# Performance work log

Measured on AMD Instinct MI355X. Metric: run time of the kernel, lower is better.

## Reference

```python
import jax, jax.numpy as jnp
import numpy as np

DIM = 96          # adapter bottleneck dim
K = 3             # conv kernel size

def quick_gelu(x):
    return x * jax.nn.sigmoid(1.702 * x)

def setup_inputs() -> dict:
    key = jax.random.key(0)
    ks = jax.random.split(key, 12)
    B, H, W, C = 64, 28, 28, 384
    x   = jax.random.normal(ks[0], (B, H, W, C), jnp.float32)
    # adapter down/up (xavier-ish scale for down; up is zero-init in the
    # original but we use small random so gradients flow in tests)
    Wd  = jax.random.normal(ks[1], (C, DIM), jnp.float32) * 0.05
    bd  = jnp.zeros((DIM,), jnp.float32)
    Wu  = jax.random.normal(ks[2], (DIM, C), jnp.float32) * 0.02
    bu  = jnp.zeros((C,), jnp.float32)
    # meta_net: Linear(C,64) -> ReLU -> Linear(64,64)
    Wm1 = jax.random.normal(ks[3], (C, 64), jnp.float32) * 0.05
    bm1 = jnp.zeros((64,), jnp.float32)
    Wm2 = jax.random.normal(ks[4], (64, 64), jnp.float32) * 0.1
    bm2 = jnp.zeros((64,), jnp.float32)
    # conv hypernet: Linear(64, DIM*DIM*K*K)
    Wh  = jax.random.normal(ks[5], (64, DIM * DIM * K * K), jnp.float32) * 0.01
    bh  = jnp.zeros((DIM * DIM * K * K,), jnp.float32)
    # learned layer embedding
    emb = jax.random.normal(ks[6], (64,), jnp.float32)
    return {"x": x, "Wd": Wd, "bd": bd, "Wm1": Wm1, "bm1": bm1,
            "Wm2": Wm2, "bm2": bm2, "Wh": Wh, "bh": bh, "emb": emb,
            "Wu": Wu, "bu": bu}

def reference(x, Wd, bd, Wm1, bm1, Wm2, bm2, Wh, bh, emb, Wu, bu):
    B, H, W, C = x.shape
    # meta_net(x) then mean over spatial dims -> per-sample prompt feature [B,64]
    h = jax.nn.relu(jnp.einsum('bhwc,cd->bhwd', x, Wm1) + bm1)
    prompt = jnp.mean(jnp.einsum('bhwd,de->bhwe', h, Wm2) + bm2, axis=(1, 2))  # [B,64]
    # hypernet: per-sample dynamic conv weights (fuse_type='add')
    wflat = (emb[None, :] + prompt) @ Wh + bh                 # [B, DIM*DIM*9]
    wconv = wflat.reshape(B * DIM, DIM, K, K)                 # grouped OIHW
    # adapter down + QuickGELU
    xd = quick_gelu(jnp.einsum('bhwc,cd->bhwd', x, Wd) + bd)  # [B,H,W,DIM]
    # fused batched dynamic conv via grouped conv (groups = B)
    xg = xd.transpose(0, 3, 1, 2).reshape(1, B * DIM, H, W)   # [1,B*DIM,H,W]
    yg = jax.lax.conv_general_dilated(
        xg, wconv, window_strides=(1, 1), padding=((1, 1), (1, 1)),
        dimension_numbers=('NCHW', 'OIHW', 'NCHW'), feature_group_count=B)
    y = yg.reshape(B, DIM, H, W).transpose(0, 2, 3, 1)        # [B,H,W,DIM]
    y = quick_gelu(y)  # dropout is identity in eval mode
    return jnp.einsum('bhwd,dc->bhwc', y, Wu) + bu
```

## Files before the change

kernel.cpp:

```cpp
#include <hip/hip_runtime.h>
#include <hip/hip_fp16.h>

#define BATCH 64
#define HH    28
#define WW2   28
#define HWPX  784
#define PTOT  50176
#define CIN   384
#define DIM   96
#define MDIM  64
#define JTOT  82944
#define WSAMP 82944

#define XD_OFF 0u
#define Y_OFF  9633792u
#define WP_OFF 19267584u
#define HS_OFF 29884416u
#define Z_OFF  29900800u
#define WUT_OFF 29917184u

typedef _Float16 f16x8 __attribute__((ext_vector_type(8)));
typedef _Float16 f16x4 __attribute__((ext_vector_type(4)));
typedef float f32x4 __attribute__((ext_vector_type(4)));

__device__ __forceinline__ float qgelu(float v) {
    return v / (1.f + __expf(-1.702f * v));
}

__global__ void k0_wcvt(const float* __restrict__ Wm1,
                        const float* __restrict__ Wd,
                        const float* __restrict__ Wu,
                        _Float16* __restrict__ Wt,
                        _Float16* __restrict__ WuT)
{
    int i = blockIdx.x * 256 + threadIdx.x;
    if (i < 61440) {
        int o = i / CIN, k = i - o * CIN;
        float v = (o < MDIM) ? Wm1[k * MDIM + o] : Wd[k * DIM + (o - MDIM)];
        Wt[i] = (_Float16)v;
    } else {
        int j = i - 61440;
        int c = j / DIM, d = j - c * DIM;
        WuT[j] = (_Float16)Wu[d * CIN + c];
    }
}

__global__ __launch_bounds__(512, 4) void k1_mfma(
    const float* __restrict__ x, const _Float16* __restrict__ Wt,
    const float* __restrict__ bm1, const float* __restrict__ bd,
    float* __restrict__ hsum, __half* __restrict__ xd)
{
    __shared__ char smem[25088];
    _Float16* xds = (_Float16*)smem;
    float*   hred = (float*)(smem + 24576);

    const int t = threadIdx.x;
    const int p0 = blockIdx.x * 128;
    const int lane = t & 63, w = t >> 6;
    const int wm = w >> 1, wn = w & 1;
    const int rl = lane & 15, q = lane >> 4;

    const float* a0 = x + (size_t)(p0 + wm * 32 + rl) * CIN + q * 8;
    const float* a1 = a0 + 16 * CIN;
    const _Float16* bp0 = Wt + (wn * 80 + rl) * CIN + q * 8;

    f32x4 acc[2][5];
    #pragma unroll
    for (int mf = 0; mf < 2; ++mf)
        #pragma unroll
        for (int nf = 0; nf < 5; ++nf) acc[mf][nf] = (f32x4){0.f, 0.f, 0.f, 0.f};

    #pragma unroll
    for (int kc = 0; kc < 12; ++kc) {
        f16x8 bv[5];
        #pragma unroll
        for (int nf = 0; nf < 5; ++nf)
            bv[nf] = *(const f16x8*)(bp0 + nf * 16 * CIN + kc * 32);

        float4 fa0 = *(const float4*)(a0 + kc * 32);
        float4 fa1 = *(const float4*)(a0 + kc * 32 + 4);
        float4 fb0 = *(const float4*)(a1 + kc * 32);
        float4 fb1 = *(const float4*)(a1 + kc * 32 + 4);

        f16x8 av[2];
        av[0][0] = (_Float16)fa0.x; av[0][1] = (_Float16)fa0.y;
        av[0][2] = (_Float16)fa0.z; av[0][3] = (_Float16)fa0.w;
        av[0][4] = (_Float16)fa1.x; av[0][5] = (_Float16)fa1.y;
        av[0][6] = (_Float16)fa1.z; av[0][7] = (_Float16)fa1.w;
        av[1][0] = (_Float16)fb0.x; av[1][1] = (_Float16)fb0.y;
        av[1][2] = (_Float16)fb0.z; av[1][3] = (_Float16)fb0.w;
        av[1][4] = (_Float16)fb1.x; av[1][5] = (_Float16)fb1.y;
        av[1][6] = (_Float16)fb1.z; av[1][7] = (_Float16)fb1.w;

        #pragma unroll
        for (int mf = 0; mf < 2; ++mf)
            #pragma unroll
            for (int nf = 0; nf < 5; ++nf)
                acc[mf][nf] = __builtin_amdgcn_mfma_f32_16x16x32_f16(
                    av[mf], bv[nf], acc[mf][nf], 0, 0, 0);
    }

    if (t < 128) hred[t] = 0.f;
    __syncthreads();

    const int s0 = p0 / HWPX, s_last = (p0 + 127) / HWPX;
    #pragma unroll
    for (int mf = 0; mf < 2; ++mf) {
        #pragma unroll
        for (int nf = 0; nf < 5; ++nf) {
            const int col = wn * 80 + nf * 16 + rl;
            #pragma unroll
            for (int j = 0; j < 4; ++j) {
                const int rr = wm * 32 + mf * 16 + q * 4 + j;
                float v = acc[mf][nf][j];
                if (col < 64) {
                    v = fmaxf(v + bm1[col], 0.f);
                    int sloc = (p0 + rr) / HWPX - s0;
                    atomicAdd(&hred[sloc * 64 + col], v);
                } else {
                    int e = col - 64;
                    xds[rr * 96 + e] = (_Float16)qgelu(v + bd[e]);
                }
            }
        }
    }
    __syncthreads();

    if (t < 128) {
        int sloc = t >> 6, col = t & 63, s = s0 + sloc;
        if (s <= s_last) atomicAdd(&hsum[s * 64 + col], hred[t]);
    }
    #pragma unroll
    for (int i = 0; i < 3; ++i) {
        int e = t + i * 512;
        *(uint4*)((__half*)xd + (size_t)p0 * 96 + e * 8) = *(uint4*)(xds + e * 8);
    }
}

__global__ void k2a_prompt(const float* __restrict__ hsum,
                           const float* __restrict__ Wm2,
                           const float* __restrict__ bm2,
                           const float* __restrict__ emb,
                           float* __restrict__ z)
{
    int idx = blockIdx.x * 256 + threadIdx.x;
    int b = idx >> 6, m = idx & 63;
    float acc = 0.f;
    #pragma unroll 8
    for (int d = 0; d < 64; ++d) acc += hsum[b * 64 + d] * Wm2[d * 64 + m];
    z[idx] = emb[m] + acc * (1.f / 784.f) + bm2[m];
}

__global__ __launch_bounds__(256) void k2b_hyper(
    const float* __restrict__ z, const float* __restrict__ Wh,
    const float* __restrict__ bh, __half* __restrict__ wperm)
{
    __shared__ float zs[4096];
    const int t = threadIdx.x;
    for (int idx = t; idx < 4096; idx += 256) zs[idx] = z[idx];
    const int j = blockIdx.x * 256 + t;
    float wh[64];
    #pragma unroll 8
    for (int m = 0; m < 64; ++m) wh[m] = Wh[(size_t)m * JTOT + j];
    __syncthreads();

    const int o = j / 864, rem = j % 864;
    const int i = rem / 9, t9 = rem % 9;
    const int base = o * 864 + t9 * 96 + i;
    const float bj = bh[j];
    for (int b = 0; b < 64; ++b) {
        float a = bj;
        const float4* zz = (const float4*)(zs + b * 64);
        #pragma unroll
        for (int m4 = 0; m4 < 16; ++m4) {
            float4 v = zz[m4];
            a += v.x * wh[4 * m4] + v.y * wh[4 * m4 + 1] +
                 v.z * wh[4 * m4 + 2] + v.w * wh[4 * m4 + 3];
        }
        wperm[(size_t)b * WSAMP + base] = __float2half(a);
    }
}

__global__ __launch_bounds__(256) void k3_mfma(
    const __half* __restrict__ xd, const __half* __restrict__ wperm,
    __half* __restrict__ y)
{
    __shared__ __half sm[17600];
    const int t = threadIdx.x;

    const int n = blockIdx.x;
    const int xcd = n & 7, jj0 = n >> 3;
    const int b = xcd * 8 + jj0 / 7;
    const int rt = jj0 % 7;
    const int h0 = rt * 4;

    if (t < 16) *(uint4*)(sm + 17472 + t * 8) = uint4{0u, 0u, 0u, 0u};
    for (int idx = t; idx < 2016; idx += 256) {
        int pix = idx / 12, q = idx - pix * 12;
        int r = pix / 28, col = pix - r * 28;
        int g = h0 - 1 + r;
        uint4 v = {0u, 0u, 0u, 0u};
        if ((unsigned)g < 28u)
            v = *(const uint4*)(xd + (size_t)(b * HWPX + g * 28 + col) * 96 + q * 8);
        *(uint4*)(sm + pix * 104 + q * 8) = v;
    }
    __syncthreads();

    const int lane = t & 63, w = t >> 6;
    const int wm = w >> 1, wn = w & 1;
    const int mloc = lane & 15, klo = (lane >> 4) * 8;
    const int base_m = wm * 64;

    int oh_[4], ow_[4]; bool pv[4];
    #pragma unroll
    for (int mf = 0; mf < 4; ++mf) {
        int p = base_m + mf * 16 + mloc;
        pv[mf] = (p < 112);
        int pp = pv[mf] ? p : 0;
        oh_[mf] = pp / 28; ow_[mf] = pp - oh_[mf] * 28;
    }
    const __half* wp = wperm + (size_t)b * WSAMP + (wn * 48 + mloc) * 864 + klo;

    f32x4 acc[4][3];
    #pragma unroll
    for (int mf = 0; mf < 4; ++mf)
        #pragma unroll
        for (int nf = 0; nf < 3; ++nf) acc[mf][nf] = (f32x4){0.f, 0.f, 0.f, 0.f};

    #pragma unroll
    for (int kh = 0; kh < 3; ++kh) {
        #pragma unroll
        for (int kw = 0; kw < 3; ++kw) {
            const int t9 = kh * 3 + kw;
            int abase[4];
            #pragma unroll
            for (int mf = 0; mf < 4; ++mf) {
                int iw = ow_[mf] + kw - 1;
                bool valid = pv[mf] && ((unsigned)iw < 28u);
                abase[mf] = valid ? ((oh_[mf] + kh) * 28 + iw) * 104 + klo
                                  : 17472 + klo;
            }
            #pragma unroll
            for (int ic = 0; ic < 3; ++ic) {
                f16x8 av[4], bv[3];
                #pragma unroll
                for (int nf = 0; nf < 3; ++nf)
                    bv[nf] = *(const f16x8*)(wp + nf * 13824 + t9 * 96 + ic * 32);
                #pragma unroll
                for (int mf = 0; mf < 4; ++mf)
                    av[mf] = *(const f16x8*)(sm + abase[mf] + ic * 32);
                #pragma unroll
                for (int mf = 0; mf < 4; ++mf)
                    #pragma unroll
                    for (int nf = 0; nf < 3; ++nf)
                        acc[mf][nf] = __builtin_amdgcn_mfma_f32_16x16x32_f16(
                            av[mf], bv[nf], acc[mf][nf], 0, 0, 0);
            }
        }
    }
    __syncthreads();

    #pragma unroll
    for (int mf = 0; mf < 4; ++mf) {
        #pragma unroll
        for (int nf = 0; nf < 3; ++nf) {
            const int o = wn * 48 + nf * 16 + mloc;
            #pragma unroll
            for (int j = 0; j < 4; ++j) {
                int p = base_m + mf * 16 + (lane >> 4) * 4 + j;
                if (p < 112)
                    sm[p * 104 + o] = __float2half(qgelu(acc[mf][nf][j]));
            }
        }
    }
    __syncthreads();
    for (int idx = t; idx < 1344; idx += 256) {
        int pix = idx / 12, q = idx - pix * 12;
        *(uint4*)(y + (size_t)(b * HWPX + h0 * 28 + pix) * 96 + q * 8) =
            *(uint4*)(sm + pix * 104 + q * 8);
    }
}

__global__ __launch_bounds__(512, 2) void k4_mfma(
    const __half* __restrict__ y, const _Float16* __restrict__ WuT,
    const float* __restrict__ bu, float* __restrict__ out)
{
    __shared__ __half ys[128 * 104];
    const int t = threadIdx.x;
    const int p0 = blockIdx.x * 128;

    #pragma unroll
    for (int i = 0; i < 3; ++i) {
        int idx = t + i * 512;
        int pix = idx / 12, q = idx - pix * 12;
        *(uint4*)(ys + pix * 104 + q * 8) =
            *(const uint4*)(y + (size_t)(p0 + pix) * 96 + q * 8);
    }

    const int lane = t & 63, w = t >> 6;
    const int wm = w >> 2, wn = w & 3;
    const int mloc = lane & 15, klo = (lane >> 4) * 8;

    float bcol[6];
    #pragma unroll
    for (int nf = 0; nf < 6; ++nf) bcol[nf] = bu[wn * 96 + nf * 16 + mloc];
    __syncthreads();

    f32x4 acc[4][6];
    #pragma unroll
    for (int mf = 0; mf < 4; ++mf)
        #pragma unroll
        for (int nf = 0; nf < 6; ++nf) acc[mf][nf] = (f32x4){0.f, 0.f, 0.f, 0.f};

    #pragma unroll
    for (int kc = 0; kc < 3; ++kc) {
        f16x8 av[4], bv[6];
        #pragma unroll
        for (int nf = 0; nf < 6; ++nf)
            bv[nf] = *(const f16x8*)(WuT + (wn * 96 + nf * 16 + mloc) * 96 + kc * 32 + klo);
        #pragma unroll
        for (int mf = 0; mf < 4; ++mf)
            av[mf] = *(const f16x8*)(ys + (wm * 64 + mf * 16 + mloc) * 104 + kc * 32 + klo);
        #pragma unroll
        for (int mf = 0; mf < 4; ++mf)
            #pragma unroll
            for (int nf = 0; nf < 6; ++nf)
                acc[mf][nf] = __builtin_amdgcn_mfma_f32_16x16x32_f16(
                    av[mf], bv[nf], acc[mf][nf], 0, 0, 0);
    }

    #pragma unroll
    for (int mf = 0; mf < 4; ++mf) {
        #pragma unroll
        for (int nf = 0; nf < 6; ++nf) {
            const int c = wn * 96 + nf * 16 + mloc;
            #pragma unroll
            for (int j = 0; j < 4; ++j) {
                int p = p0 + wm * 64 + mf * 16 + (lane >> 4) * 4 + j;
                out[(size_t)p * CIN + c] = acc[mf][nf][j] + bcol[nf];
            }
        }
    }
}

extern "C" void kernel_launch(void* const* d_in, const int* in_sizes, int n_in,
                              void* d_out, int out_size, void* d_ws, size_t ws_size,
                              hipStream_t stream)
{
    const float* x   = (const float*)d_in[0];
    const float* Wd  = (const float*)d_in[1];
    const float* bd  = (const float*)d_in[2];
    const float* Wm1 = (const float*)d_in[3];
    const float* bm1 = (const float*)d_in[4];
    const float* Wm2 = (const float*)d_in[5];
    const float* bm2 = (const float*)d_in[6];
    const float* Wh  = (const float*)d_in[7];
    const float* bh  = (const float*)d_in[8];
    const float* emb = (const float*)d_in[9];
    const float* Wu  = (const float*)d_in[10];
    const float* bu  = (const float*)d_in[11];
    float* out = (float*)d_out;

    char* ws = (char*)d_ws;
    __half*   xd    = (__half*)(ws + XD_OFF);
    __half*   ybuf  = (__half*)(ws + Y_OFF);
    __half*   wperm = (__half*)(ws + WP_OFF);
    float*    hsum  = (float*)(ws + HS_OFF);
    float*    z     = (float*)(ws + Z_OFF);
    _Float16* Wt    = (_Float16*)(ws + WP_OFF);
    _Float16* WuT   = (_Float16*)(ws + WUT_OFF);

    hipMemsetAsync(hsum, 0, 64 * 64 * sizeof(float), stream);

    k0_wcvt<<<384, 256, 0, stream>>>(Wm1, Wd, Wu, Wt, WuT);
    k1_mfma<<<392, 512, 0, stream>>>(x, Wt, bm1, bd, hsum, xd);
    k2a_prompt<<<16, 256, 0, stream>>>(hsum, Wm2, bm2, emb, z);
    k2b_hyper<<<324, 256, 0, stream>>>(z, Wh, bh, wperm);
    k3_mfma<<<448, 256, 0, stream>>>(xd, wperm, ybuf);
    k4_mfma<<<392, 512, 0, stream>>>(ybuf, WuT, bu, out);
}
```

Measured before the change: 167.9 us.

## Stage k1 GEMM operands through double-buffered LDS with 64-row tiles

The first projection kernel (x times Wm1/Wd) now copies A and B chunks into padded, double-buffered shared memory tiles, prefetching the chunk two steps ahead into registers. Before, each wave read its operands directly from global memory. The block also shrinks from 512 to 256 threads and covers 64 pixels, so twice as many blocks are launched. The aim is to share weight loads across waves and hide global latency, at the cost of extra LDS traffic and a barrier on each k-step.

```diff
diff --git a/kernel.cpp b/kernel.cpp
--- a/kernel.cpp
+++ b/kernel.cpp
@@ -45,24 +45,57 @@
     }
 }
 
-__global__ __launch_bounds__(512, 4) void k1_mfma(
+__global__ __launch_bounds__(256) void k1_mfma(
     const float* __restrict__ x, const _Float16* __restrict__ Wt,
     const float* __restrict__ bm1, const float* __restrict__ bd,
     float* __restrict__ hsum, __half* __restrict__ xd)
 {
-    __shared__ char smem[25088];
+    __shared__ char smem[32768];
+    _Float16* As  = (_Float16*)smem;
+    _Float16* Bs  = (_Float16*)(smem + 9216);
+    float*   hred = (float*)(smem + 32256);
     _Float16* xds = (_Float16*)smem;
-    float*   hred = (float*)(smem + 24576);
 
     const int t = threadIdx.x;
-    const int p0 = blockIdx.x * 128;
+    const int p0 = blockIdx.x * 64;
     const int lane = t & 63, w = t >> 6;
     const int wm = w >> 1, wn = w & 1;
     const int rl = lane & 15, q = lane >> 4;
 
-    const float* a0 = x + (size_t)(p0 + wm * 32 + rl) * CIN + q * 8;
-    const float* a1 = a0 + 16 * CIN;
-    const _Float16* bp0 = Wt + (wn * 80 + rl) * CIN + q * 8;
+    const int arow = t >> 2, acol = (t & 3) * 8;
+    const int brow0 = t >> 2;
+    const int brow1 = (t + 256) >> 2;
+    const int brow2 = (t + 512) >> 2;
+    const int bcol = (t & 3) * 8;
+
+    const float*    ag  = x  + (size_t)(p0 + arow) * CIN + acol;
+    const _Float16* bg0 = Wt + brow0 * CIN + bcol;
+    const _Float16* bg1 = Wt + brow1 * CIN + bcol;
+    const _Float16* bg2 = Wt + brow2 * CIN + bcol;
+
+    float4 ra[2][2];
+    uint4  rb[2][3];
+
+#define LOAD_CHUNK(s, kc_) do {                                   \
+    ra[s][0] = *(const float4*)(ag + (kc_) * 32);                 \
+    ra[s][1] = *(const float4*)(ag + (kc_) * 32 + 4);             \
+    rb[s][0] = *(const uint4*)(bg0 + (kc_) * 32);                 \
+    rb[s][1] = *(const uint4*)(bg1 + (kc_) * 32);                 \
+    if (t < 128) rb[s][2] = *(const uint4*)(bg2 + (kc_) * 32);    \
+} while (0)
+
+#define WRITE_CHUNK(s) do {                                       \
+    f16x8 h;                                                      \
+    h[0] = (_Float16)ra[s][0].x; h[1] = (_Float16)ra[s][0].y;     \
+    h[2] = (_Float16)ra[s][0].z; h[3] = (_Float16)ra[s][0].w;     \
+    h[4] = (_Float16)ra[s][1].x; h[5] = (_Float16)ra[s][1].y;     \
+    h[6] = (_Float16)ra[s][1].z; h[7] = (_Float16)ra[s][1].w;     \
+    *(f16x8*)(As + (s) * 2304 + arow * 36 + acol) = h;            \
+    *(uint4*)(Bs + (s) * 5760 + brow0 * 36 + bcol) = rb[s][0];    \
+    *(uint4*)(Bs + (s) * 5760 + brow1 * 36 + bcol) = rb[s][1];    \
+    if (t < 128)                                                  \
+        *(uint4*)(Bs + (s) * 5760 + brow2 * 36 + bcol) = rb[s][2];\
+} while (0)
 
     f32x4 acc[2][5];
     #pragma unroll
@@ -70,27 +103,23 @@
         #pragma unroll
         for (int nf = 0; nf < 5; ++nf) acc[mf][nf] = (f32x4){0.f, 0.f, 0.f, 0.f};
 
+    LOAD_CHUNK(0, 0);
+    WRITE_CHUNK(0);
+    LOAD_CHUNK(1, 1);
+    __syncthreads();
+
     #pragma unroll
     for (int kc = 0; kc < 12; ++kc) {
-        f16x8 bv[5];
+        const int cur = kc & 1;
+
+        f16x8 av[2], bv[5];
+        av[0] = *(f16x8*)(As + cur * 2304 + (wm * 32 + rl) * 36 + q * 8);
+        av[1] = *(f16x8*)(As + cur * 2304 + (wm * 32 + 16 + rl) * 36 + q * 8);
         #pragma unroll
         for (int nf = 0; nf < 5; ++nf)
-            bv[nf] = *(const f16x8*)(bp0 + nf * 16 * CIN + kc * 32);
-
-        float4 fa0 = *(const float4*)(a0 + kc * 32);
-        float4 fa1 = *(const float4*)(a0 + kc * 32 + 4);
-        float4 fb0 = *(const float4*)(a1 + kc * 32);
-        float4 fb1 = *(const float4*)(a1 + kc * 32 + 4);
-
-        f16x8 av[2];
-        av[0][0] = (_Float16)fa0.x; av[0][1] = (_Float16)fa0.y;
-        av[0][2] = (_Float16)fa0.z; av[0][3] = (_Float16)fa0.w;
-        av[0][4] = (_Float16)fa1.x; av[0][5] = (_Float16)fa1.y;
-        av[0][6] = (_Float16)fa1.z; av[0][7] = (_Float16)fa1.w;
-        av[1][0] = (_Float16)fb0.x; av[1][1] = (_Float16)fb0.y;
-        av[1][2] = (_Float16)fb0.z; av[1][3] = (_Float16)fb0.w;
-        av[1][4] = (_Float16)fb1.x; av[1][5] = (_Float16)fb1.y;
-        av[1][6] = (_Float16)fb1.z; av[1][7] = (_Float16)fb1.w;
+            bv[nf] = *(f16x8*)(Bs + cur * 5760 + (wn * 80 + nf * 16 + rl) * 36 + q * 8);
+
+        if (kc + 2 < 12) LOAD_CHUNK(cur, kc + 2);
 
         #pragma unroll
         for (int mf = 0; mf < 2; ++mf)
@@ -98,12 +127,20 @@
             for (int nf = 0; nf < 5; ++nf)
                 acc[mf][nf] = __builtin_amdgcn_mfma_f32_16x16x32_f16(
                     av[mf], bv[nf], acc[mf][nf], 0, 0, 0);
-    }
-
+
+        if (kc + 1 < 12) {
+            WRITE_CHUNK(cur ^ 1);
+            __syncthreads();
+        }
+    }
+#undef LOAD_CHUNK
+#undef WRITE_CHUNK
+
+    __syncthreads();
     if (t < 128) hred[t] = 0.f;
     __syncthreads();
 
-    const int s0 = p0 / HWPX, s_last = (p0 + 127) / HWPX;
+    const int s0 = p0 / HWPX, s_last = (p0 + 63) / HWPX;
     #pragma unroll
     for (int mf = 0; mf < 2; ++mf) {
         #pragma unroll
@@ -132,7 +169,7 @@
     }
     #pragma unroll
     for (int i = 0; i < 3; ++i) {
-        int e = t + i * 512;
+        int e = t + i * 256;
         *(uint4*)((__half*)xd + (size_t)p0 * 96 + e * 8) = *(uint4*)(xds + e * 8);
     }
 }
@@ -373,7 +410,7 @@
     hipMemsetAsync(hsum, 0, 64 * 64 * sizeof(float), stream);
 
     k0_wcvt<<<384, 256, 0, stream>>>(Wm1, Wd, Wu, Wt, WuT);
-    k1_mfma<<<392, 512, 0, stream>>>(x, Wt, bm1, bd, hsum, xd);
+    k1_mfma<<<784, 256, 0, stream>>>(x, Wt, bm1, bd, hsum, xd);
     k2a_prompt<<<16, 256, 0, stream>>>(hsum, Wm2, bm2, emb, z);
     k2b_hyper<<<324, 256, 0, stream>>>(z, Wh, bh, wperm);
     k3_mfma<<<448, 256, 0, stream>>>(xd, wperm, ybuf);
```

After: 181.1 us. 7.9% more time.

## Stage k1 GEMM operands through double-buffered LDS and split N across blocks

Applied to the files above, without the earlier changes.

Restructures the first projection GEMM so that A (x, converted to fp16) and B tiles are staged through double-buffered shared memory, with a three-deep register prefetch of global loads. The old version loaded operands straight from global into registers. The 160 output columns are now split across two blocks per 128-row tile, doubling the grid to 784 blocks so each wave does one M fragment. The aim is better memory latency hiding and occupancy. The cost is that each x tile is now read twice (once per column half) and there is a barrier on every k-step.

```diff
diff --git a/kernel.cpp b/kernel.cpp
--- a/kernel.cpp
+++ b/kernel.cpp
@@ -50,90 +50,122 @@
     const float* __restrict__ bm1, const float* __restrict__ bd,
     float* __restrict__ hsum, __half* __restrict__ xd)
 {
-    __shared__ char smem[25088];
+    __shared__ char smem[30464];
+    _Float16* As  = (_Float16*)smem;
+    _Float16* Bs  = (_Float16*)(smem + 18432);
+    float*   hred = (float*)(smem + 29952);
     _Float16* xds = (_Float16*)smem;
-    float*   hred = (float*)(smem + 24576);
 
     const int t = threadIdx.x;
-    const int p0 = blockIdx.x * 128;
+    const int bid = blockIdx.x;
+    const int mt = bid >> 1, nb = bid & 1;
+    const int p0 = mt * 128;
+    const int ncol0 = nb * 80;
+
     const int lane = t & 63, w = t >> 6;
-    const int wm = w >> 1, wn = w & 1;
     const int rl = lane & 15, q = lane >> 4;
 
-    const float* a0 = x + (size_t)(p0 + wm * 32 + rl) * CIN + q * 8;
-    const float* a1 = a0 + 16 * CIN;
-    const _Float16* bp0 = Wt + (wn * 80 + rl) * CIN + q * 8;
-
-    f32x4 acc[2][5];
-    #pragma unroll
-    for (int mf = 0; mf < 2; ++mf)
-        #pragma unroll
-        for (int nf = 0; nf < 5; ++nf) acc[mf][nf] = (f32x4){0.f, 0.f, 0.f, 0.f};
+    const int arow = t >> 2, acol = (t & 3) * 8;
+    const float* ag = x + (size_t)(p0 + arow) * CIN + acol;
+    const bool bact = (t < 320);
+    const int brow = t >> 2, bcol = (t & 3) * 8;
+    const _Float16* bg = Wt + (size_t)(ncol0 + (bact ? brow : 0)) * CIN + bcol;
+
+    float4 ra[3][2];
+    uint4  rb[3];
+
+#define LOADC(s, kc_) do {                                        \
+    ra[s][0] = *(const float4*)(ag + (kc_) * 32);                 \
+    ra[s][1] = *(const float4*)(ag + (kc_) * 32 + 4);             \
+    if (bact) rb[s] = *(const uint4*)(bg + (kc_) * 32);           \
+} while (0)
+
+#define WRITEC(buf, s) do {                                       \
+    f16x8 h;                                                      \
+    h[0] = (_Float16)ra[s][0].x; h[1] = (_Float16)ra[s][0].y;     \
+    h[2] = (_Float16)ra[s][0].z; h[3] = (_Float16)ra[s][0].w;     \
+    h[4] = (_Float16)ra[s][1].x; h[5] = (_Float16)ra[s][1].y;     \
+    h[6] = (_Float16)ra[s][1].z; h[7] = (_Float16)ra[s][1].w;     \
+    *(f16x8*)(As + (buf) * 4608 + arow * 36 + acol) = h;          \
+    if (bact)                                                     \
+        *(uint4*)(Bs + (buf) * 2880 + brow * 36 + bcol) = rb[s];  \
+} while (0)
+
+    f32x4 acc[5];
+    #pragma unroll
+    for (int nf = 0; nf < 5; ++nf) acc[nf] = (f32x4){0.f, 0.f, 0.f, 0.f};
+
+    LOADC(0, 0); LOADC(1, 1); LOADC(2, 2);
+    WRITEC(0, 0);
+    __syncthreads();
 
     #pragma unroll
     for (int kc = 0; kc < 12; ++kc) {
+        const int cur = kc & 1;
+
+        f16x8 av = *(f16x8*)(As + cur * 4608 + (w * 16 + rl) * 36 + q * 8);
         f16x8 bv[5];
         #pragma unroll
         for (int nf = 0; nf < 5; ++nf)
-            bv[nf] = *(const f16x8*)(bp0 + nf * 16 * CIN + kc * 32);
-
-        float4 fa0 = *(const float4*)(a0 + kc * 32);
-        float4 fa1 = *(const float4*)(a0 + kc * 32 + 4);
-        float4 fb0 = *(const float4*)(a1 + kc * 32);
-        float4 fb1 = *(const float4*)(a1 + kc * 32 + 4);
-
-        f16x8 av[2];
-        av[0][0] = (_Float16)fa0.x; av[0][1] = (_Float16)fa0.y;
-        av[0][2] = (_Float16)fa0.z; av[0][3] = (_Float16)fa0.w;
-        av[0][4] = (_Float16)fa1.x; av[0][5] = (_Float16)fa1.y;
-        av[0][6] = (_Float16)fa1.z; av[0][7] = (_Float16)fa1.w;
-        av[1][0] = (_Float16)fb0.x; av[1][1] = (_Float16)fb0.y;
-        av[1][2] = (_Float16)fb0.z; av[1][3] = (_Float16)fb0.w;
-        av[1][4] = (_Float16)fb1.x; av[1][5] = (_Float16)fb1.y;
-        av[1][6] = (_Float16)fb1.z; av[1][7] = (_Float16)fb1.w;
-
-        #pragma unroll
-        for (int mf = 0; mf < 2; ++mf)
-            #pragma unroll
-            for (int nf = 0; nf < 5; ++nf)
-                acc[mf][nf] = __builtin_amdgcn_mfma_f32_16x16x32_f16(
-                    av[mf], bv[nf], acc[mf][nf], 0, 0, 0);
-    }
-
+            bv[nf] = *(f16x8*)(Bs + cur * 2880 + (nf * 16 + rl) * 36 + q * 8);
+
+        if (kc + 3 < 12) LOADC(kc % 3, kc + 3);
+
+        #pragma unroll
+        for (int nf = 0; nf < 5; ++nf)
+            acc[nf] = __builtin_amdgcn_mfma_f32_16x16x32_f16(
+                av, bv[nf], acc[nf], 0, 0, 0);
+
+        if (kc + 1 < 12) {
+            WRITEC(cur ^ 1, (kc + 1) % 3);
+            __syncthreads();
+        }
+    }
+#undef LOADC
+#undef WRITEC
+
+    __syncthreads();
     if (t < 128) hred[t] = 0.f;
     __syncthreads();
 
     const int s0 = p0 / HWPX, s_last = (p0 + 127) / HWPX;
     #pragma unroll
-    for (int mf = 0; mf < 2; ++mf) {
-        #pragma unroll
-        for (int nf = 0; nf < 5; ++nf) {
-            const int col = wn * 80 + nf * 16 + rl;
-            #pragma unroll
-            for (int j = 0; j < 4; ++j) {
-                const int rr = wm * 32 + mf * 16 + q * 4 + j;
-                float v = acc[mf][nf][j];
-                if (col < 64) {
-                    v = fmaxf(v + bm1[col], 0.f);
-                    int sloc = (p0 + rr) / HWPX - s0;
-                    atomicAdd(&hred[sloc * 64 + col], v);
-                } else {
-                    int e = col - 64;
-                    xds[rr * 96 + e] = (_Float16)qgelu(v + bd[e]);
-                }
+    for (int nf = 0; nf < 5; ++nf) {
+        const int col = ncol0 + nf * 16 + rl;
+        #pragma unroll
+        for (int j = 0; j < 4; ++j) {
+            const int rr = w * 16 + q * 4 + j;
+            float v = acc[nf][j];
+            if (nb == 0 && col < 64) {
+                v = fmaxf(v + bm1[col], 0.f);
+                int sloc = (p0 + rr) / HWPX - s0;
+                atomicAdd(&hred[sloc * 64 + col], v);
+            } else {
+                int e = col - 64;
+                float g = qgelu(v + bd[e]);
+                if (nb == 0) xds[rr * 16 + (e)] = (_Float16)g;
+                else         xds[rr * 80 + (e - 16)] = (_Float16)g;
             }
         }
     }
     __syncthreads();
 
-    if (t < 128) {
-        int sloc = t >> 6, col = t & 63, s = s0 + sloc;
-        if (s <= s_last) atomicAdd(&hsum[s * 64 + col], hred[t]);
-    }
-    #pragma unroll
-    for (int i = 0; i < 3; ++i) {
-        int e = t + i * 512;
-        *(uint4*)((__half*)xd + (size_t)p0 * 96 + e * 8) = *(uint4*)(xds + e * 8);
+    if (nb == 0) {
+        if (t < 128) {
+            int sloc = t >> 6, col = t & 63, s = s0 + sloc;
+            if (s <= s_last) atomicAdd(&hsum[s * 64 + col], hred[t]);
+        }
+        if (t < 256) {
+            int row = t >> 1, h8 = t & 1;
+            *(uint4*)((__half*)xd + (size_t)(p0 + row) * 96 + h8 * 8) =
+                *(uint4*)(xds + row * 16 + h8 * 8);
+        }
+    } else {
+        for (int idx = t; idx < 1280; idx += 512) {
+            int row = idx / 10, q10 = idx - row * 10;
+            *(uint4*)((__half*)xd + (size_t)(p0 + row) * 96 + 16 + q10 * 8) =
+                *(uint4*)(xds + row * 80 + q10 * 8);
+        }
     }
 }
 
@@ -373,7 +405,7 @@
     hipMemsetAsync(hsum, 0, 64 * 64 * sizeof(float), stream);
 
     k0_wcvt<<<384, 256, 0, stream>>>(Wm1, Wd, Wu, Wt, WuT);
-    k1_mfma<<<392, 512, 0, stream>>>(x, Wt, bm1, bd, hsum, xd);
+    k1_mfma<<<784, 512, 0, stream>>>(x, Wt, bm1, bd, hsum, xd);
     k2a_prompt<<<16, 256, 0, stream>>>(hsum, Wm2, bm2, emb, z);
     k2b_hyper<<<324, 256, 0, stream>>>(z, Wh, bh, wperm);
     k3_mfma<<<448, 256, 0, stream>>>(xd, wperm, ybuf);
```

Result: slower. 225.4 us (+34.3%).

## Stage k1 GEMM operands through double-buffered LDS with register prefetch

Applied to the files above, without the earlier changes.

The down-projection GEMM kernel used to load the x rows and fp16 weights straight from global memory into MFMA fragments. It now loads each tile once per block with coalesced reads, converts x to fp16, and writes both operands into padded, double-buffered shared memory. Loads run two k-chunks ahead in registers. This cuts redundant global weight reads across warps and overlaps memory with compute, at the cost of larger LDS use, a lower occupancy hint (2 instead of 4), and a barrier per k-step.

```diff
diff --git a/kernel.cpp b/kernel.cpp
--- a/kernel.cpp
+++ b/kernel.cpp
@@ -45,14 +45,16 @@
     }
 }
 
-__global__ __launch_bounds__(512, 4) void k1_mfma(
+__global__ __launch_bounds__(512, 2) void k1_mfma(
     const float* __restrict__ x, const _Float16* __restrict__ Wt,
     const float* __restrict__ bm1, const float* __restrict__ bd,
     float* __restrict__ hsum, __half* __restrict__ xd)
 {
-    __shared__ char smem[25088];
+    __shared__ char smem[46592];
+    _Float16* As  = (_Float16*)smem;
+    _Float16* Bs  = (_Float16*)(smem + 20480);
+    float*   hred = (float*)(smem + 46080);
     _Float16* xds = (_Float16*)smem;
-    float*   hred = (float*)(smem + 24576);
 
     const int t = threadIdx.x;
     const int p0 = blockIdx.x * 128;
@@ -60,9 +62,36 @@
     const int wm = w >> 1, wn = w & 1;
     const int rl = lane & 15, q = lane >> 4;
 
-    const float* a0 = x + (size_t)(p0 + wm * 32 + rl) * CIN + q * 8;
-    const float* a1 = a0 + 16 * CIN;
-    const _Float16* bp0 = Wt + (wn * 80 + rl) * CIN + q * 8;
+    const int ar0 = t >> 3, aq0 = t & 7;
+    const int br0 = t >> 2, bq0 = t & 3;
+
+    const float*    ag0 = x + (size_t)(p0 + ar0) * CIN + aq0 * 4;
+    const float*    ag1 = ag0 + (size_t)64 * CIN;
+    const _Float16* bg0 = Wt + br0 * CIN + bq0 * 8;
+    const _Float16* bg1 = Wt + (br0 + 128) * CIN + bq0 * 8;
+
+    float4 ra[2][2];
+    uint4  rb[2][2];
+
+#define LOADC(s, kc_) do {                                        \
+    ra[s][0] = *(const float4*)(ag0 + (kc_) * 32);                \
+    ra[s][1] = *(const float4*)(ag1 + (kc_) * 32);                \
+    rb[s][0] = *(const uint4*)(bg0 + (kc_) * 32);                 \
+    if (t < 128) rb[s][1] = *(const uint4*)(bg1 + (kc_) * 32);    \
+} while (0)
+
+#define WRITEC(buf, s) do {                                       \
+    f16x4 h0, h1;                                                 \
+    h0[0] = (_Float16)ra[s][0].x; h0[1] = (_Float16)ra[s][0].y;   \
+    h0[2] = (_Float16)ra[s][0].z; h0[3] = (_Float16)ra[s][0].w;   \
+    h1[0] = (_Float16)ra[s][1].x; h1[1] = (_Float16)ra[s][1].y;   \
+    h1[2] = (_Float16)ra[s][1].z; h1[3] = (_Float16)ra[s][1].w;   \
+    *(f16x4*)(As + (buf) * 5120 + ar0 * 40 + aq0 * 4) = h0;       \
+    *(f16x4*)(As + (buf) * 5120 + (ar0 + 64) * 40 + aq0 * 4) = h1;\
+    *(uint4*)(Bs + (buf) * 6400 + br0 * 40 + bq0 * 8) = rb[s][0]; \
+    if (t < 128)                                                  \
+        *(uint4*)(Bs + (buf) * 6400 + (br0 + 128) * 40 + bq0 * 8) = rb[s][1]; \
+} while (0)
 
     f32x4 acc[2][5];
     #pragma unroll
@@ -70,27 +99,23 @@
         #pragma unroll
         for (int nf = 0; nf < 5; ++nf) acc[mf][nf] = (f32x4){0.f, 0.f, 0.f, 0.f};
 
+    LOADC(0, 0);
+    LOADC(1, 1);
+    WRITEC(0, 0);
+    __syncthreads();
+
     #pragma unroll
     for (int kc = 0; kc < 12; ++kc) {
-        f16x8 bv[5];
+        const int cur = kc & 1;
+
+        f16x8 av[2], bv[5];
+        av[0] = *(f16x8*)(As + cur * 5120 + (wm * 32 + rl) * 40 + q * 8);
+        av[1] = *(f16x8*)(As + cur * 5120 + (wm * 32 + 16 + rl) * 40 + q * 8);
         #pragma unroll
         for (int nf = 0; nf < 5; ++nf)
-            bv[nf] = *(const f16x8*)(bp0 + nf * 16 * CIN + kc * 32);
-
-        float4 fa0 = *(const float4*)(a0 + kc * 32);
-        float4 fa1 = *(const float4*)(a0 + kc * 32 + 4);
-        float4 fb0 = *(const float4*)(a1 + kc * 32);
-        float4 fb1 = *(const float4*)(a1 + kc * 32 + 4);
-
-        f16x8 av[2];
-        av[0][0] = (_Float16)fa0.x; av[0][1] = (_Float16)fa0.y;
-        av[0][2] = (_Float16)fa0.z; av[0][3] = (_Float16)fa0.w;
-        av[0][4] = (_Float16)fa1.x; av[0][5] = (_Float16)fa1.y;
-        av[0][6] = (_Float16)fa1.z; av[0][7] = (_Float16)fa1.w;
-        av[1][0] = (_Float16)fb0.x; av[1][1] = (_Float16)fb0.y;
-        av[1][2] = (_Float16)fb0.z; av[1][3] = (_Float16)fb0.w;
-        av[1][4] = (_Float16)fb1.x; av[1][5] = (_Float16)fb1.y;
-        av[1][6] = (_Float16)fb1.z; av[1][7] = (_Float16)fb1.w;
+            bv[nf] = *(f16x8*)(Bs + cur * 6400 + (wn * 80 + nf * 16 + rl) * 40 + q * 8);
+
+        if (kc + 2 < 12) LOADC(kc & 1, kc + 2);
 
         #pragma unroll
         for (int mf = 0; mf < 2; ++mf)
@@ -98,7 +123,14 @@
             for (int nf = 0; nf < 5; ++nf)
                 acc[mf][nf] = __builtin_amdgcn_mfma_f32_16x16x32_f16(
                     av[mf], bv[nf], acc[mf][nf], 0, 0, 0);
-    }
+
+        if (kc + 1 < 12) {
+            WRITEC(cur ^ 1, (kc + 1) & 1);
+            __syncthreads();
+        }
+    }
+#undef LOADC
+#undef WRITEC
 
     if (t < 128) hred[t] = 0.f;
     __syncthreads();
```

Measured after the change: 151.1 us. 10.0% less time.
